# Performance work log

Hardware: AMD Instinct MI355X
Metric: run time of the kernel (lower is better)

Reference implementation:

```python
import jax, jax.numpy as jnp
import numpy as np

N, E, B, T_IN = 10000, 160000, 8, 12
HP, HV = 64, 32        # p_model_hid_dim, v_model_hid_dim (hardcoded in __init__)
TIME_UNITS = 10.0


def layernorm(x, g, b, eps=1e-5):
    m = jnp.mean(x, axis=-1, keepdims=True)
    v = jnp.var(x, axis=-1, keepdims=True)
    return (x - m) / jnp.sqrt(v + eps) * g + b


def setup_inputs() -> dict:
    key = jax.random.key(0)
    ks = jax.random.split(key, 30)

    def lin(k, out_d, in_d):
        return jax.random.normal(k, (out_d, in_d), jnp.float32) / np.sqrt(in_d)

    inp = {
        "feature": jax.random.normal(ks[0], (N, B, T_IN), jnp.float32),
        "upstream": jax.random.uniform(ks[1], (E, B, T_IN), jnp.float32),
        "downstream": jax.random.uniform(ks[2], (E, B, T_IN), jnp.float32),
        "distance": jax.random.uniform(ks[3], (E,), jnp.float32) * 200.0,
        "src": jax.random.randint(ks[4], (E,), 0, N, jnp.int32),
        "dst": jax.random.randint(ks[5], (E,), 0, N, jnp.int32),
        # learned edge parameter (init ~U(0,1) to avoid clamp boundary)
        "alpha": jax.random.uniform(ks[6], (E, 1), jnp.float32),
        # Probabilistic_Model params
        "fc_w": lin(ks[7], HP, T_IN),                       # Linear(T_in, HP, bias=False)
        "ln2_g": jnp.ones((2 * HP + 1,), jnp.float32),
        "ln2_b": jnp.zeros((2 * HP + 1,), jnp.float32),
        "attn_w": lin(ks[8], 1, 2 * HP + 1),                # Linear(2HP+1, 1, bias=False)
        # Velocity_Model_NAM params
        "l11_w": lin(ks[9], HV, T_IN), "l11_b": jnp.zeros((HV,), jnp.float32),
        "ln11_g": jnp.ones((HV,), jnp.float32), "ln11_b": jnp.zeros((HV,), jnp.float32),
        "l12_w": lin(ks[10], 1, HV), "l12_b": jnp.zeros((1,), jnp.float32),
        "l21_w": lin(ks[11], HV, T_IN), "l21_b": jnp.zeros((HV,), jnp.float32),
        "ln21_g": jnp.ones((HV,), jnp.float32), "ln21_b": jnp.zeros((HV,), jnp.float32),
        "l22_w": lin(ks[12], 1, HV), "l22_b": jnp.zeros((1,), jnp.float32),
        "l3_w": lin(ks[13], 1, 3), "l3_b": jnp.zeros((1,), jnp.float32),
    }
    return inp


def reference(feature, upstream, downstream, distance, alpha,
              fc_w, ln2_g, ln2_b, attn_w,
              l11_w, l11_b, ln11_g, ln11_b, l12_w, l12_b,
              l21_w, l21_b, ln21_g, ln21_b, l22_w, l22_b,
              l3_w, l3_b, src, dst):
    # node embeddings: [N, B, HP]
    z = jnp.einsum('nbt,ht->nbh', feature, fc_w)

    # ---- Velocity_Model_NAM (dropout is identity in eval) ----
    x_up = jax.nn.relu(layernorm(jnp.einsum('ebt,ht->ebh', upstream, l11_w) + l11_b, ln11_g, ln11_b))
    x_up = jax.nn.sigmoid(jnp.einsum('ebh,oh->ebo', x_up, l12_w) + l12_b)        # [E,B,1]
    x_dn = jax.nn.relu(layernorm(jnp.einsum('ebt,ht->ebh', downstream, l21_w) + l21_b, ln21_g, ln21_b))
    x_dn = jax.nn.sigmoid(jnp.einsum('ebh,oh->ebo', x_dn, l22_w) + l22_b)        # [E,B,1]
    t_rep = jnp.broadcast_to(alpha[:, None, :], (alpha.shape[0], x_up.shape[1], 1))
    x = jnp.concatenate([x_up, x_dn, t_rep], axis=2)                              # [E,B,3]
    v = jax.nn.softplus(jnp.einsum('ebc,oc->ebo', x, l3_w) + l3_b)[..., 0]        # [E,B]
    v = jnp.minimum(v, 3.0)

    # travel time per edge/batch: [E,B]
    T = distance[:, None] / (v + 1e-5)
    T_idx = jnp.clip(jnp.round(T / TIME_UNITS), 0.0, T_IN - 1.0)

    # ---- per-edge diffusion power series (vectorized) ----
    # F[e,b] * (1-F[e,b])^(n-1-k) for k < n, else 0;  n = T_IN - T_idx
    F = 1.0 / (1.0 + jnp.clip(alpha, 0.0, 1.0) * T)                               # [E,B]
    n = T_IN - T_idx                                                              # [E,B]
    k = jnp.arange(T_IN, dtype=T.dtype)
    expo = n[..., None] - 1.0 - k                                                 # [E,B,T]
    diff = jnp.where(expo >= 0.0,
                     F[..., None] * jnp.power(1.0 - F[..., None], jnp.maximum(expo, 0.0)),
                     0.0)

    # ---- edge attention, softmax grouped by src node ----
    zc = jnp.concatenate([z[src], z[dst], jax.lax.stop_gradient(T)[..., None]], axis=2)  # [E,B,2HP+1]
    a = jnp.einsum('ebc,oc->ebo', layernorm(zc, ln2_g, ln2_b), attn_w)[..., 0]    # [E,B]
    a = jax.nn.leaky_relu(a, 0.01)
    amax = jax.ops.segment_max(a, src, num_segments=N)                            # [N,B]
    ex = jnp.exp(a - amax[src])
    den = jax.ops.segment_sum(ex, src, num_segments=N)
    e = ex / den[src]                                                             # [E,B]

    # ---- message + reduce (scatter-sum over dst) ----
    msg = e * jnp.sum(diff * feature[src], axis=2)                                # [E,B]
    pred = jax.ops.segment_sum(msg, dst, num_segments=N)                          # [N,B]
    return pred
```

## Files before the change

kernel.cpp:

```cpp
#include <hip/hip_runtime.h>
#include <math.h>

#define NN 10000
#define NE 160000
#define NB 8
#define TT 12
#define HP 64
#define HV 32

#define WS_FLOATS (NN * NB * 4 + NE * NB + NN * NB + 4)
#define WS_F4 ((WS_FLOATS) / 4)

typedef float v2 __attribute__((ext_vector_type(2)));

__device__ __forceinline__ v2 fma2(v2 a, v2 b, v2 c) { return __builtin_elementwise_fma(a, b, c); }

__device__ __forceinline__ void load_row12v(const float* __restrict__ p, v2* r2) {
  const float4* p4 = reinterpret_cast<const float4*>(p);
  float4 a = p4[0], b = p4[1], c = p4[2];
  r2[0] = (v2){a.x, a.y}; r2[1] = (v2){a.z, a.w};
  r2[2] = (v2){b.x, b.y}; r2[3] = (v2){b.z, b.w};
  r2[4] = (v2){c.x, c.y}; r2[5] = (v2){c.z, c.w};
}

__device__ __forceinline__ void load_row12(const float* __restrict__ p, float* row) {
  const float4* p4 = reinterpret_cast<const float4*>(p);
  float4 r0 = p4[0], r1 = p4[1], r2 = p4[2];
  row[0]=r0.x; row[1]=r0.y; row[2]=r0.z; row[3]=r0.w;
  row[4]=r1.x; row[5]=r1.y; row[6]=r1.z; row[7]=r1.w;
  row[8]=r2.x; row[9]=r2.y; row[10]=r2.z; row[11]=r2.w;
}

__global__ __launch_bounds__(256) void k_init(float4* __restrict__ ws4, float4* __restrict__ pred4) {
  unsigned i = blockIdx.x * 256 + threadIdx.x;
  float4 z; z.x = 0.f; z.y = 0.f; z.z = 0.f; z.w = 0.f;
  for (unsigned j = i; j < (unsigned)WS_F4; j += 256u * 1024u) ws4[j] = z;
  if (i < NN * NB / 4) pred4[i] = z;
}

__global__ __launch_bounds__(256) void k_node(const float* __restrict__ feature,
                                              const float* __restrict__ fc_w,
                                              const float* __restrict__ attn_w,
                                              const float* __restrict__ ln2_g,
                                              const float* __restrict__ ln2_b,
                                              float4* __restrict__ nodeAgg,
                                              float* __restrict__ consts) {
  if (blockIdx.x == 0) {
    __shared__ float r1[256], r2[256];
    int c = threadIdx.x;
    float vg = 0.f, vb = 0.f;
    if (c < 2 * HP + 1) {
      float aw = attn_w[c];
      vg = aw * ln2_g[c];
      vb = aw * ln2_b[c];
    }
    r1[c] = vg; r2[c] = vb;
    __syncthreads();
    for (int off = 128; off > 0; off >>= 1) {
      if (c < off) { r1[c] += r1[c + off]; r2[c] += r2[c + off]; }
      __syncthreads();
    }
    if (c == 0) {
      consts[0] = r1[0];
      consts[1] = r2[0];
      consts[2] = attn_w[2 * HP] * ln2_g[2 * HP];
      consts[3] = 0.f;
    }
  }

  int t = blockIdx.x * 256 + threadIdx.x;
  if (t >= NN * NB) return;
  v2 row2[6];
  load_row12v(feature + (size_t)t * TT, row2);
  const v2* wv  = reinterpret_cast<const v2*>(fc_w);
  const v2* awv = reinterpret_cast<const v2*>(attn_w);
  const v2* gv  = reinterpret_cast<const v2*>(ln2_g);
  v2 A1p = {0.f,0.f}, A2p = {0.f,0.f}, Dsp = {0.f,0.f}, Ddp = {0.f,0.f};
#pragma unroll
  for (int c2 = 0; c2 < HP / 2; ++c2) {
    v2 a0 = {0.f,0.f}, a1 = {0.f,0.f};
#pragma unroll
    for (int k2 = 0; k2 < 6; ++k2) {
      a0 = fma2(row2[k2], wv[(2 * c2) * 6 + k2], a0);
      a1 = fma2(row2[k2], wv[(2 * c2 + 1) * 6 + k2], a1);
    }
    v2 zp = {a0.x + a0.y, a1.x + a1.y};
    A1p += zp;
    A2p = fma2(zp, zp, A2p);
    v2 wgs = awv[c2] * gv[c2];
    v2 wgd = awv[HP / 2 + c2] * gv[HP / 2 + c2];
    Dsp = fma2(wgs, zp, Dsp);
    Ddp = fma2(wgd, zp, Ddp);
  }
  float4 o;
  o.x = A1p.x + A1p.y; o.y = A2p.x + A2p.y; o.z = Dsp.x + Dsp.y; o.w = Ddp.x + Ddp.y;
  nodeAgg[t] = o;
}

__device__ __forceinline__ float nam_branch(const v2* row2, const float* __restrict__ w,
                                            const float* __restrict__ bias,
                                            const float* __restrict__ g,
                                            const float* __restrict__ bb,
                                            const float* __restrict__ w2, float b2) {
  const v2* wv    = reinterpret_cast<const v2*>(w);
  const v2* biasv = reinterpret_cast<const v2*>(bias);
  const v2* gv    = reinterpret_cast<const v2*>(g);
  const v2* bbv   = reinterpret_cast<const v2*>(bb);
  const v2* w2v   = reinterpret_cast<const v2*>(w2);
  v2 hp[HV / 2];
  v2 sp1 = {0.f,0.f}, sp2 = {0.f,0.f};
#pragma unroll
  for (int j2 = 0; j2 < HV / 2; ++j2) {
    v2 a0 = {0.f,0.f}, a1 = {0.f,0.f};
#pragma unroll
    for (int k2 = 0; k2 < 6; ++k2) {
      a0 = fma2(row2[k2], wv[(2 * j2) * 6 + k2], a0);
      a1 = fma2(row2[k2], wv[(2 * j2 + 1) * 6 + k2], a1);
    }
    v2 bp = biasv[j2];
    v2 h = {a0.x + a0.y + bp.x, a1.x + a1.y + bp.y};
    hp[j2] = h;
    sp1 += h;
    sp2 = fma2(h, h, sp2);
  }
  float s1 = sp1.x + sp1.y, s2 = sp2.x + sp2.y;
  float m = s1 * (1.f / HV);
  float var = s2 * (1.f / HV) - m * m;
  float inv = rsqrtf(var + 1e-5f);
  v2 inv2 = {inv, inv};
  float nmi = -m * inv;
  v2 nmi2 = {nmi, nmi};
  v2 acc2 = {0.f,0.f};
  v2 zero = {0.f,0.f};
#pragma unroll
  for (int j2 = 0; j2 < HV / 2; ++j2) {
    v2 tt = fma2(hp[j2], inv2, nmi2);
    v2 y = fma2(tt, gv[j2], bbv[j2]);
    y = __builtin_elementwise_max(y, zero);
    acc2 = fma2(y, w2v[j2], acc2);
  }
  float acc = acc2.x + acc2.y + b2;
  return 1.f / (1.f + __expf(-acc));
}

__global__ __launch_bounds__(256) void k_edge1(
    const float* __restrict__ upstream, const float* __restrict__ downstream,
    const float* __restrict__ distance, const float* __restrict__ alpha,
    const int* __restrict__ src, const int* __restrict__ dst,
    const float* __restrict__ feature, const float4* __restrict__ nodeAgg,
    const float* __restrict__ l11_w, const float* __restrict__ l11_b,
    const float* __restrict__ ln11_g, const float* __restrict__ ln11_b,
    const float* __restrict__ l12_w, const float* __restrict__ l12_b,
    const float* __restrict__ l21_w, const float* __restrict__ l21_b,
    const float* __restrict__ ln21_g, const float* __restrict__ ln21_b,
    const float* __restrict__ l22_w, const float* __restrict__ l22_b,
    const float* __restrict__ l3_w, const float* __restrict__ l3_b,
    const float* __restrict__ consts,
    float* __restrict__ prod, float* __restrict__ den) {
  int t = blockIdx.x * 256 + threadIdx.x;
  int e = t >> 3, b = t & 7;
  int se = src[e], de = dst[e];

  v2 row2[6];
  load_row12v(upstream + (size_t)t * TT, row2);
  float xu = nam_branch(row2, l11_w, l11_b, ln11_g, ln11_b, l12_w, l12_b[0]);
  load_row12v(downstream + (size_t)t * TT, row2);
  float xd = nam_branch(row2, l21_w, l21_b, ln21_g, ln21_b, l22_w, l22_b[0]);

  float al = alpha[e];
  float vp = fmaf(l3_w[0], xu, fmaf(l3_w[1], xd, fmaf(l3_w[2], al, l3_b[0])));
  float v = fmaxf(vp, 0.f) + log1pf(__expf(-fabsf(vp)));
  v = fminf(v, 3.f);
  float Tt = distance[e] / (v + 1e-5f);
  float Ti = fminf(fmaxf(rintf(Tt * 0.1f), 0.f), (float)(TT - 1));
  int n = TT - (int)Ti;
  float acl = fminf(fmaxf(al, 0.f), 1.f);
  float F = 1.f / (1.f + acl * Tt);
  float omF = 1.f - F;

  float row[TT];
  load_row12(feature + ((size_t)se * NB + b) * TT, row);
  float pw = 1.f, s = 0.f;
#pragma unroll
  for (int k = TT - 1; k >= 0; --k) {
    if (k <= n - 1) { s = fmaf(pw, row[k], s); pw *= omF; }
  }
  s *= F;

  float4 As = nodeAgg[(size_t)se * NB + b];
  float4 Ad = nodeAgg[(size_t)de * NB + b];
  float s1 = As.x + Ad.x + Tt;
  float s2 = As.y + Ad.y + Tt * Tt;
  float sd = As.z + Ad.w + consts[2] * Tt;

  float m = s1 * (1.f / 129.f);
  float var = s2 * (1.f / 129.f) - m * m;
  float inv = rsqrtf(var + 1e-5f);
  float a = fmaf(inv, sd - m * consts[0], consts[1]);
  a = (a >= 0.f) ? a : 0.01f * a;

  float ex = __expf(a);
  prod[t] = ex * s;
  atomicAdd(&den[(size_t)se * NB + b], ex);
}

__global__ __launch_bounds__(256) void k_edge2(const int* __restrict__ src,
                                               const int* __restrict__ dst,
                                               const float* __restrict__ prod,
                                               const float* __restrict__ den,
                                               float* __restrict__ pred) {
  int t = blockIdx.x * 256 + threadIdx.x;
  int e = t >> 3, b = t & 7;
  float p = prod[t] / den[(size_t)src[e] * NB + b];
  atomicAdd(&pred[(size_t)dst[e] * NB + b], p);
}

extern "C" void kernel_launch(void* const* d_in, const int* in_sizes, int n_in,
                              void* d_out, int out_size, void* d_ws, size_t ws_size,
                              hipStream_t stream) {
  const float* feature   = (const float*)d_in[0];
  const float* upstream  = (const float*)d_in[1];
  const float* downstream= (const float*)d_in[2];
  const float* distance  = (const float*)d_in[3];
  const int*   src       = (const int*)d_in[4];
  const int*   dst       = (const int*)d_in[5];
  const float* alpha     = (const float*)d_in[6];
  const float* fc_w      = (const float*)d_in[7];
  const float* ln2_g     = (const float*)d_in[8];
  const float* ln2_b     = (const float*)d_in[9];
  const float* attn_w    = (const float*)d_in[10];
  const float* l11_w     = (const float*)d_in[11];
  const float* l11_b     = (const float*)d_in[12];
  const float* ln11_g    = (const float*)d_in[13];
  const float* ln11_b    = (const float*)d_in[14];
  const float* l12_w     = (const float*)d_in[15];
  const float* l12_b     = (const float*)d_in[16];
  const float* l21_w     = (const float*)d_in[17];
  const float* l21_b     = (const float*)d_in[18];
  const float* ln21_g    = (const float*)d_in[19];
  const float* ln21_b    = (const float*)d_in[20];
  const float* l22_w     = (const float*)d_in[21];
  const float* l22_b     = (const float*)d_in[22];
  const float* l3_w      = (const float*)d_in[23];
  const float* l3_b      = (const float*)d_in[24];
  float* pred = (float*)d_out;

  float* ws = (float*)d_ws;
  float4* nodeAgg = (float4*)ws;
  float* prod   = ws + (size_t)NN * NB * 4;
  float* den    = prod + (size_t)NE * NB;
  float* consts = den + (size_t)NN * NB;

  k_init<<<1024, 256, 0, stream>>>((float4*)ws, (float4*)pred);
  k_node<<<(NN * NB + 255) / 256, 256, 0, stream>>>(feature, fc_w, attn_w, ln2_g, ln2_b,
                                                    nodeAgg, consts);

  int eb = NE * NB;
  k_edge1<<<eb / 256, 256, 0, stream>>>(upstream, downstream, distance, alpha, src, dst,
                                        feature, nodeAgg,
                                        l11_w, l11_b, ln11_g, ln11_b, l12_w, l12_b,
                                        l21_w, l21_b, ln21_g, ln21_b, l22_w, l22_b,
                                        l3_w, l3_b, consts, prod, den);
  k_edge2<<<eb / 256, 256, 0, stream>>>(src, dst, prod, den, pred);
}
```

Baseline: 240.8 us.

## Fuse all stages into one persistent kernel with software grid barriers

```diff
diff --git a/kernel.cpp b/kernel.cpp
--- a/kernel.cpp
+++ b/kernel.cpp
@@ -8,8 +8,11 @@
 #define HP 64
 #define HV 32
 
-#define WS_FLOATS (NN * NB * 4 + NE * NB + NN * NB + 4)
-#define WS_F4 ((WS_FLOATS) / 4)
+#define NBLK 1536
+#define NTHR 256
+#define GRID_T (NBLK * NTHR)
+#define EB (NE * NB)
+#define NITER 4
 
 typedef float v2 __attribute__((ext_vector_type(2)));
 
@@ -31,70 +34,23 @@
   row[8]=r2.x; row[9]=r2.y; row[10]=r2.z; row[11]=r2.w;
 }
 
-__global__ __launch_bounds__(256) void k_init(float4* __restrict__ ws4, float4* __restrict__ pred4) {
-  unsigned i = blockIdx.x * 256 + threadIdx.x;
-  float4 z; z.x = 0.f; z.y = 0.f; z.z = 0.f; z.w = 0.f;
-  for (unsigned j = i; j < (unsigned)WS_F4; j += 256u * 1024u) ws4[j] = z;
-  if (i < NN * NB / 4) pred4[i] = z;
-}
-
-__global__ __launch_bounds__(256) void k_node(const float* __restrict__ feature,
-                                              const float* __restrict__ fc_w,
-                                              const float* __restrict__ attn_w,
-                                              const float* __restrict__ ln2_g,
-                                              const float* __restrict__ ln2_b,
-                                              float4* __restrict__ nodeAgg,
-                                              float* __restrict__ consts) {
-  if (blockIdx.x == 0) {
-    __shared__ float r1[256], r2[256];
-    int c = threadIdx.x;
-    float vg = 0.f, vb = 0.f;
-    if (c < 2 * HP + 1) {
-      float aw = attn_w[c];
-      vg = aw * ln2_g[c];
-      vb = aw * ln2_b[c];
-    }
-    r1[c] = vg; r2[c] = vb;
-    __syncthreads();
-    for (int off = 128; off > 0; off >>= 1) {
-      if (c < off) { r1[c] += r1[c + off]; r2[c] += r2[c + off]; }
-      __syncthreads();
-    }
-    if (c == 0) {
-      consts[0] = r1[0];
-      consts[1] = r2[0];
-      consts[2] = attn_w[2 * HP] * ln2_g[2 * HP];
-      consts[3] = 0.f;
-    }
-  }
-
-  int t = blockIdx.x * 256 + threadIdx.x;
-  if (t >= NN * NB) return;
-  v2 row2[6];
-  load_row12v(feature + (size_t)t * TT, row2);
-  const v2* wv  = reinterpret_cast<const v2*>(fc_w);
-  const v2* awv = reinterpret_cast<const v2*>(attn_w);
-  const v2* gv  = reinterpret_cast<const v2*>(ln2_g);
-  v2 A1p = {0.f,0.f}, A2p = {0.f,0.f}, Dsp = {0.f,0.f}, Ddp = {0.f,0.f};
-#pragma unroll
-  for (int c2 = 0; c2 < HP / 2; ++c2) {
-    v2 a0 = {0.f,0.f}, a1 = {0.f,0.f};
-#pragma unroll
-    for (int k2 = 0; k2 < 6; ++k2) {
-      a0 = fma2(row2[k2], wv[(2 * c2) * 6 + k2], a0);
-      a1 = fma2(row2[k2], wv[(2 * c2 + 1) * 6 + k2], a1);
-    }
-    v2 zp = {a0.x + a0.y, a1.x + a1.y};
-    A1p += zp;
-    A2p = fma2(zp, zp, A2p);
-    v2 wgs = awv[c2] * gv[c2];
-    v2 wgd = awv[HP / 2 + c2] * gv[HP / 2 + c2];
-    Dsp = fma2(wgs, zp, Dsp);
-    Ddp = fma2(wgd, zp, Ddp);
-  }
-  float4 o;
-  o.x = A1p.x + A1p.y; o.y = A2p.x + A2p.y; o.z = Dsp.x + Dsp.y; o.w = Ddp.x + Ddp.y;
-  nodeAgg[t] = o;
+__device__ __forceinline__ void gridbar(unsigned* bar) {
+  __syncthreads();
+  if (threadIdx.x == 0) {
+    __threadfence();
+    unsigned prev = __hip_atomic_fetch_add(bar, 1u, __ATOMIC_ACQ_REL, __HIP_MEMORY_SCOPE_AGENT);
+    if (prev + 1u < (unsigned)NBLK) {
+      while (__hip_atomic_load(bar, __ATOMIC_ACQUIRE, __HIP_MEMORY_SCOPE_AGENT) < (unsigned)NBLK)
+        __builtin_amdgcn_s_sleep(8);
+    }
+    __threadfence();
+  }
+  __syncthreads();
+}
+
+__global__ void k_init(unsigned* __restrict__ bars) {
+  if (threadIdx.x < 2)
+    __hip_atomic_store(&bars[threadIdx.x], 0u, __ATOMIC_RELEASE, __HIP_MEMORY_SCOPE_AGENT);
 }
 
 __device__ __forceinline__ float nam_branch(const v2* row2, const float* __restrict__ w,
@@ -143,11 +99,12 @@
   return 1.f / (1.f + __expf(-acc));
 }
 
-__global__ __launch_bounds__(256) void k_edge1(
-    const float* __restrict__ upstream, const float* __restrict__ downstream,
-    const float* __restrict__ distance, const float* __restrict__ alpha,
-    const int* __restrict__ src, const int* __restrict__ dst,
-    const float* __restrict__ feature, const float4* __restrict__ nodeAgg,
+__global__ __launch_bounds__(NTHR, 6) void k_main(
+    const float* __restrict__ feature, const float* __restrict__ upstream,
+    const float* __restrict__ downstream, const float* __restrict__ distance,
+    const float* __restrict__ alpha, const int* __restrict__ src, const int* __restrict__ dst,
+    const float* __restrict__ fc_w, const float* __restrict__ ln2_g, const float* __restrict__ ln2_b,
+    const float* __restrict__ attn_w,
     const float* __restrict__ l11_w, const float* __restrict__ l11_b,
     const float* __restrict__ ln11_g, const float* __restrict__ ln11_b,
     const float* __restrict__ l12_w, const float* __restrict__ l12_b,
@@ -155,64 +112,130 @@
     const float* __restrict__ ln21_g, const float* __restrict__ ln21_b,
     const float* __restrict__ l22_w, const float* __restrict__ l22_b,
     const float* __restrict__ l3_w, const float* __restrict__ l3_b,
-    const float* __restrict__ consts,
-    float* __restrict__ prod, float* __restrict__ den) {
-  int t = blockIdx.x * 256 + threadIdx.x;
-  int e = t >> 3, b = t & 7;
-  int se = src[e], de = dst[e];
-
-  v2 row2[6];
-  load_row12v(upstream + (size_t)t * TT, row2);
-  float xu = nam_branch(row2, l11_w, l11_b, ln11_g, ln11_b, l12_w, l12_b[0]);
-  load_row12v(downstream + (size_t)t * TT, row2);
-  float xd = nam_branch(row2, l21_w, l21_b, ln21_g, ln21_b, l22_w, l22_b[0]);
-
-  float al = alpha[e];
-  float vp = fmaf(l3_w[0], xu, fmaf(l3_w[1], xd, fmaf(l3_w[2], al, l3_b[0])));
-  float v = fmaxf(vp, 0.f) + log1pf(__expf(-fabsf(vp)));
-  v = fminf(v, 3.f);
-  float Tt = distance[e] / (v + 1e-5f);
-  float Ti = fminf(fmaxf(rintf(Tt * 0.1f), 0.f), (float)(TT - 1));
-  int n = TT - (int)Ti;
-  float acl = fminf(fmaxf(al, 0.f), 1.f);
-  float F = 1.f / (1.f + acl * Tt);
-  float omF = 1.f - F;
-
-  float row[TT];
-  load_row12(feature + ((size_t)se * NB + b) * TT, row);
-  float pw = 1.f, s = 0.f;
-#pragma unroll
-  for (int k = TT - 1; k >= 0; --k) {
-    if (k <= n - 1) { s = fmaf(pw, row[k], s); pw *= omF; }
-  }
-  s *= F;
-
-  float4 As = nodeAgg[(size_t)se * NB + b];
-  float4 Ad = nodeAgg[(size_t)de * NB + b];
-  float s1 = As.x + Ad.x + Tt;
-  float s2 = As.y + Ad.y + Tt * Tt;
-  float sd = As.z + Ad.w + consts[2] * Tt;
-
-  float m = s1 * (1.f / 129.f);
-  float var = s2 * (1.f / 129.f) - m * m;
-  float inv = rsqrtf(var + 1e-5f);
-  float a = fmaf(inv, sd - m * consts[0], consts[1]);
-  a = (a >= 0.f) ? a : 0.01f * a;
-
-  float ex = __expf(a);
-  prod[t] = ex * s;
-  atomicAdd(&den[(size_t)se * NB + b], ex);
-}
-
-__global__ __launch_bounds__(256) void k_edge2(const int* __restrict__ src,
-                                               const int* __restrict__ dst,
-                                               const float* __restrict__ prod,
-                                               const float* __restrict__ den,
-                                               float* __restrict__ pred) {
-  int t = blockIdx.x * 256 + threadIdx.x;
-  int e = t >> 3, b = t & 7;
-  float p = prod[t] / den[(size_t)src[e] * NB + b];
-  atomicAdd(&pred[(size_t)dst[e] * NB + b], p);
+    float4* __restrict__ nodeAgg, float* __restrict__ den, float* __restrict__ consts,
+    float* __restrict__ prodArr, unsigned* __restrict__ bars, float* __restrict__ pred) {
+  int t0 = blockIdx.x * NTHR + threadIdx.x;
+
+  if (blockIdx.x == 0) {
+    __shared__ float r1[NTHR], r2[NTHR];
+    int c = threadIdx.x;
+    float vg = 0.f, vb = 0.f;
+    if (c < 2 * HP + 1) {
+      float aw = attn_w[c];
+      vg = aw * ln2_g[c];
+      vb = aw * ln2_b[c];
+    }
+    r1[c] = vg; r2[c] = vb;
+    __syncthreads();
+    for (int off = 128; off > 0; off >>= 1) {
+      if (c < off) { r1[c] += r1[c + off]; r2[c] += r2[c + off]; }
+      __syncthreads();
+    }
+    if (c == 0) {
+      consts[0] = r1[0];
+      consts[1] = r2[0];
+      consts[2] = attn_w[2 * HP] * ln2_g[2 * HP];
+    }
+  }
+
+  if (t0 < NN * NB) {
+    den[t0] = 0.f;
+    pred[t0] = 0.f;
+    v2 row2[6];
+    load_row12v(feature + (size_t)t0 * TT, row2);
+    const v2* wv  = reinterpret_cast<const v2*>(fc_w);
+    const v2* awv = reinterpret_cast<const v2*>(attn_w);
+    const v2* gv  = reinterpret_cast<const v2*>(ln2_g);
+    v2 A1p = {0.f,0.f}, A2p = {0.f,0.f}, Dsp = {0.f,0.f}, Ddp = {0.f,0.f};
+#pragma unroll
+    for (int c2 = 0; c2 < HP / 2; ++c2) {
+      v2 a0 = {0.f,0.f}, a1 = {0.f,0.f};
+#pragma unroll
+      for (int k2 = 0; k2 < 6; ++k2) {
+        a0 = fma2(row2[k2], wv[(2 * c2) * 6 + k2], a0);
+        a1 = fma2(row2[k2], wv[(2 * c2 + 1) * 6 + k2], a1);
+      }
+      v2 zp = {a0.x + a0.y, a1.x + a1.y};
+      A1p += zp;
+      A2p = fma2(zp, zp, A2p);
+      v2 wgs = awv[c2] * gv[c2];
+      v2 wgd = awv[HP / 2 + c2] * gv[HP / 2 + c2];
+      Dsp = fma2(wgs, zp, Dsp);
+      Ddp = fma2(wgd, zp, Ddp);
+    }
+    float4 o;
+    o.x = A1p.x + A1p.y; o.y = A2p.x + A2p.y; o.z = Dsp.x + Dsp.y; o.w = Ddp.x + Ddp.y;
+    nodeAgg[t0] = o;
+  }
+
+  gridbar(bars + 0);
+
+  float c0 = __hip_atomic_load(&consts[0], __ATOMIC_RELAXED, __HIP_MEMORY_SCOPE_AGENT);
+  float c1 = __hip_atomic_load(&consts[1], __ATOMIC_RELAXED, __HIP_MEMORY_SCOPE_AGENT);
+  float c2 = __hip_atomic_load(&consts[2], __ATOMIC_RELAXED, __HIP_MEMORY_SCOPE_AGENT);
+
+#pragma unroll 1
+  for (int it = 0; it < NITER; ++it) {
+    int q = t0 + it * GRID_T;
+    if (q < EB) {
+      int e = q >> 3, b = q & 7;
+      int se = src[e], de = dst[e];
+
+      v2 row2[6];
+      load_row12v(upstream + (size_t)q * TT, row2);
+      float xu = nam_branch(row2, l11_w, l11_b, ln11_g, ln11_b, l12_w, l12_b[0]);
+      load_row12v(downstream + (size_t)q * TT, row2);
+      float xd = nam_branch(row2, l21_w, l21_b, ln21_g, ln21_b, l22_w, l22_b[0]);
+
+      float al = alpha[e];
+      float vp = fmaf(l3_w[0], xu, fmaf(l3_w[1], xd, fmaf(l3_w[2], al, l3_b[0])));
+      float v = fmaxf(vp, 0.f) + log1pf(__expf(-fabsf(vp)));
+      v = fminf(v, 3.f);
+      float Tt = distance[e] / (v + 1e-5f);
+      float Ti = fminf(fmaxf(rintf(Tt * 0.1f), 0.f), (float)(TT - 1));
+      int n = TT - (int)Ti;
+      float acl = fminf(fmaxf(al, 0.f), 1.f);
+      float F = 1.f / (1.f + acl * Tt);
+      float omF = 1.f - F;
+
+      float row[TT];
+      load_row12(feature + ((size_t)se * NB + b) * TT, row);
+      float pw = 1.f, s = 0.f;
+#pragma unroll
+      for (int k = TT - 1; k >= 0; --k) {
+        if (k <= n - 1) { s = fmaf(pw, row[k], s); pw *= omF; }
+      }
+      s *= F;
+
+      float4 As = nodeAgg[(size_t)se * NB + b];
+      float4 Ad = nodeAgg[(size_t)de * NB + b];
+      float s1 = As.x + Ad.x + Tt;
+      float s2 = As.y + Ad.y + Tt * Tt;
+      float sd = As.z + Ad.w + c2 * Tt;
+
+      float m = s1 * (1.f / 129.f);
+      float var = s2 * (1.f / 129.f) - m * m;
+      float inv = rsqrtf(var + 1e-5f);
+      float a = fmaf(inv, sd - m * c0, c1);
+      a = (a >= 0.f) ? a : 0.01f * a;
+
+      float ex = __expf(a);
+      prodArr[q] = ex * s;
+      atomicAdd(&den[(size_t)se * NB + b], ex);
+    }
+  }
+
+  gridbar(bars + 1);
+
+#pragma unroll 1
+  for (int it = 0; it < NITER; ++it) {
+    int q = t0 + it * GRID_T;
+    if (q < EB) {
+      int e = q >> 3, b = q & 7;
+      float p = prodArr[q] / den[(size_t)src[e] * NB + b];
+      atomicAdd(&pred[(size_t)dst[e] * NB + b], p);
+    }
+  }
 }
 
 extern "C" void kernel_launch(void* const* d_in, const int* in_sizes, int n_in,
@@ -247,19 +270,16 @@
 
   float* ws = (float*)d_ws;
   float4* nodeAgg = (float4*)ws;
-  float* prod   = ws + (size_t)NN * NB * 4;
-  float* den    = prod + (size_t)NE * NB;
-  float* consts = den + (size_t)NN * NB;
-
-  k_init<<<1024, 256, 0, stream>>>((float4*)ws, (float4*)pred);
-  k_node<<<(NN * NB + 255) / 256, 256, 0, stream>>>(feature, fc_w, attn_w, ln2_g, ln2_b,
-                                                    nodeAgg, consts);
-
-  int eb = NE * NB;
-  k_edge1<<<eb / 256, 256, 0, stream>>>(upstream, downstream, distance, alpha, src, dst,
-                                        feature, nodeAgg,
-                                        l11_w, l11_b, ln11_g, ln11_b, l12_w, l12_b,
-                                        l21_w, l21_b, ln21_g, ln21_b, l22_w, l22_b,
-                                        l3_w, l3_b, consts, prod, den);
-  k_edge2<<<eb / 256, 256, 0, stream>>>(src, dst, prod, den, pred);
-}
+  float* den     = ws + (size_t)NN * NB * 4;
+  float* consts  = den + (size_t)NN * NB;
+  float* prodArr = consts + 4;
+  unsigned* bars = (unsigned*)(prodArr + (size_t)EB);
+
+  k_init<<<1, 64, 0, stream>>>(bars);
+  k_main<<<NBLK, NTHR, 0, stream>>>(feature, upstream, downstream, distance, alpha, src, dst,
+                                    fc_w, ln2_g, ln2_b, attn_w,
+                                    l11_w, l11_b, ln11_g, ln11_b, l12_w, l12_b,
+                                    l21_w, l21_b, ln21_g, ln21_b, l22_w, l22_b,
+                                    l3_w, l3_b,
+                                    nodeAgg, den, consts, prodArr, bars, pred);
+}
```

Measured after the change: 805.4 us. 3.34x slower.
